# Optimization experiments

Measured on AMD Instinct MI355X. Metric: run time of the kernel, lower is better.

Reference implementation:

```python
import jax, jax.numpy as jnp
import numpy as np
import math

D_MODEL = 768
NUM_HEADS = 12
D_K = D_MODEL // NUM_HEADS

def setup_inputs() -> dict:
    key = jax.random.key(0)
    k_x, k_q, k_k, k_v, k_o = jax.random.split(key, 5)
    x = jax.random.normal(k_x, (2, 2048, D_MODEL), dtype=jnp.float32)
    std = math.sqrt(2.0 / (D_MODEL + D_MODEL))
    # trunc_normal approx: clip normal to [-3std, 3std]
    def tn(k):
        return jnp.clip(jax.random.normal(k, (D_MODEL, D_MODEL), dtype=jnp.float32) * std, -3 * std, 3 * std)
    return {
        "x": x,
        "weight_query": tn(k_q),
        "weight_key": tn(k_k),
        "weight_value": tn(k_v),
        "weight_output": tn(k_o),
    }

def reference(x, weight_query, weight_key, weight_value, weight_output):
    # x: (b, s, d_model); weights: (d_out, d_model)
    b, s, _ = x.shape
    def proj_heads(w):
        y = jnp.einsum('od,bsd->bso', w, x)  # (b, s, h*dk)
        return y.reshape(b, s, NUM_HEADS, D_K).transpose(0, 2, 1, 3)  # (b, h, s, dk)
    Q = proj_heads(weight_query)
    K = proj_heads(weight_key)
    V = proj_heads(weight_value)
    scores = jnp.einsum('bhqd,bhkd->bhqk', Q, K) / jnp.sqrt(jnp.asarray(D_K, x.dtype))
    causal = jnp.tril(jnp.ones((s, s), dtype=bool))  # (sq, sk)
    scores = jnp.where(causal, scores, -jnp.inf)
    attn = jax.nn.softmax(scores, axis=-1)
    out_heads = jnp.einsum('bhqk,bhkd->bhqd', attn, V)  # (b, h, s, dv)
    attn_out = out_heads.transpose(0, 2, 1, 3).reshape(b, s, NUM_HEADS * D_K)
    return jnp.einsum('di,bsi->bsd', weight_output, attn_out)
```

## Files before the change

kernel.cpp:

```cpp
#include <hip/hip_runtime.h>
#include <stdint.h>

typedef float f32x4 __attribute__((ext_vector_type(4)));
typedef __bf16 bf16x8 __attribute__((ext_vector_type(8)));
typedef uint32_t u32a  __attribute__((may_alias));
typedef uint2    u2a   __attribute__((may_alias));
typedef uint4    u4a   __attribute__((may_alias));

#define VS 2064

__device__ __forceinline__ ushort f2b(float f) {
  uint32_t u = __builtin_bit_cast(uint32_t, f);
  u += 0x7FFFu + ((u >> 16) & 1u);
  return (ushort)(u >> 16);
}
__device__ __forceinline__ uint32_t b16(uint32_t u) {
  u += 0x7FFFu + ((u >> 16) & 1u);
  return u >> 16;
}

__device__ __forceinline__ bf16x8 ld_frag(const ushort* p) {
  u4a u = *(const u4a*)p;
  return __builtin_bit_cast(bf16x8, u);
}

__device__ __forceinline__ u4a cvt8(const float* p) {
  u4a a = *(const u4a*)p, b = *(const u4a*)(p + 4), o;
  o.x = b16(a.x) | (b16(a.y) << 16);
  o.y = b16(a.z) | (b16(a.w) << 16);
  o.z = b16(b.x) | (b16(b.y) << 16);
  o.w = b16(b.z) | (b16(b.w) << 16);
  return o;
}

__device__ __forceinline__ void load_lds16(const void* g, void* l) {
  __builtin_amdgcn_global_load_lds(
      (const __attribute__((address_space(1))) uint32_t*)g,
      (__attribute__((address_space(3))) uint32_t*)l, 16, 0, 0);
}

__device__ __forceinline__ uint32_t comb2(uint32_t a, uint32_t b, float w0, float w1) {
  float lo = __builtin_bit_cast(float, a << 16) * w0 +
             __builtin_bit_cast(float, b << 16) * w1;
  float hi = __builtin_bit_cast(float, a & 0xFFFF0000u) * w0 +
             __builtin_bit_cast(float, b & 0xFFFF0000u) * w1;
  return (uint32_t)f2b(lo) | ((uint32_t)f2b(hi) << 16);
}

__global__ __launch_bounds__(256) void convert_kernel(
    const float* __restrict__ x,  const float* __restrict__ wq,
    const float* __restrict__ wk, const float* __restrict__ wv,
    const float* __restrict__ wo,
    ushort* __restrict__ xb,  ushort* __restrict__ wqb,
    ushort* __restrict__ wkb, ushort* __restrict__ wvb,
    ushort* __restrict__ wob)
{
  const size_t NX = 3145728, NW = 589824;
  size_t idx = ((size_t)blockIdx.x * 256 + threadIdx.x) * 8;
  const float* src; ushort* dst; size_t off;
  if      (idx < NX)          { src = x;  dst = xb;  off = idx; }
  else if (idx < NX + NW)     { src = wq; dst = wqb; off = idx - NX; }
  else if (idx < NX + 2 * NW) { src = wk; dst = wkb; off = idx - NX - NW; }
  else if (idx < NX + 3 * NW) { src = wv; dst = wvb; off = idx - NX - 2 * NW; }
  else                        { src = wo; dst = wob; off = idx - NX - 3 * NW; }
  *(u4a*)(dst + off) = cvt8(src + off);
}

__global__ __launch_bounds__(256) void gemm_qkv(
    const ushort* __restrict__ A,
    const ushort* __restrict__ B0, const ushort* __restrict__ B1,
    const ushort* __restrict__ B2,
    ushort* __restrict__ Qo, ushort* __restrict__ Ko, ushort* __restrict__ Vt,
    int M, int N, int K)
{
  const ushort* B = blockIdx.z == 0 ? B0 : (blockIdx.z == 1 ? B1 : B2);
  const int m0 = blockIdx.x * 128, n0 = blockIdx.y * 64;
  __shared__ ushort As[128 * 64];
  __shared__ ushort Bs[64 * 64];
  const int tid = threadIdx.x, wave = tid >> 6, lane = tid & 63;
  const int quad = lane >> 4, l16 = lane & 15;
  const int mw = (wave & 1) * 64, nw = (wave >> 1) * 32;
  f32x4 acc[4][2] = {};

  for (int k0 = 0; k0 < K; k0 += 64) {
#pragma unroll
    for (int i = 0; i < 4; ++i) {
      int c = i * 256 + tid;
      load_lds16(A + (size_t)(m0 + (c >> 3)) * K + k0 + (c & 7) * 8,
                 As + (size_t)(i * 256 + wave * 64) * 8);
    }
#pragma unroll
    for (int i = 0; i < 2; ++i) {
      int c = i * 256 + tid;
      load_lds16(B + (size_t)(n0 + (c >> 3)) * K + k0 + (c & 7) * 8,
                 Bs + (size_t)(i * 256 + wave * 64) * 8);
    }
    __syncthreads();
#pragma unroll
    for (int ks = 0; ks < 2; ++ks) {
      bf16x8 af[4], bfr[2];
#pragma unroll
      for (int i = 0; i < 4; ++i)
        af[i]  = ld_frag(As + (mw + i * 16 + l16) * 64 + ks * 32 + quad * 8);
#pragma unroll
      for (int j = 0; j < 2; ++j)
        bfr[j] = ld_frag(Bs + (nw + j * 16 + l16) * 64 + ks * 32 + quad * 8);
#pragma unroll
      for (int i = 0; i < 4; ++i)
#pragma unroll
        for (int j = 0; j < 2; ++j)
          acc[i][j] = __builtin_amdgcn_mfma_f32_16x16x32_bf16(af[i], bfr[j], acc[i][j], 0, 0, 0);
    }
    __syncthreads();
  }
  if (blockIdx.z < 2) {
    ushort* C = blockIdx.z == 0 ? Qo : Ko;
    const float sc = blockIdx.z == 0 ? 0.125f : 1.0f;
#pragma unroll
    for (int i = 0; i < 4; ++i)
#pragma unroll
      for (int j = 0; j < 2; ++j)
#pragma unroll
        for (int r = 0; r < 4; ++r) {
          int row = m0 + mw + i * 16 + quad * 4 + r;
          int col = n0 + nw + j * 16 + l16;
          C[(size_t)row * N + col] = f2b(acc[i][j][r] * sc);
        }
  } else {
#pragma unroll
    for (int i = 0; i < 4; ++i)
#pragma unroll
      for (int j = 0; j < 2; ++j) {
        int col = n0 + nw + j * 16 + l16;
        int h = col >> 6, dv = col & 63;
        int t = m0 + mw + i * 16 + quad * 4;
        int b = t >> 11, s = t & 2047;
        u2a pw;
        pw.x = (uint32_t)f2b(acc[i][j][0]) | ((uint32_t)f2b(acc[i][j][1]) << 16);
        pw.y = (uint32_t)f2b(acc[i][j][2]) | ((uint32_t)f2b(acc[i][j][3]) << 16);
        *(u2a*)(Vt + (((size_t)b * 12 + h) * 64 + dv) * VS + s) = pw;
      }
  }
}

__global__ __launch_bounds__(256) void gemm_out(
    const ushort* __restrict__ A, const ushort* __restrict__ B,
    float* __restrict__ C, int M, int N, int K)
{
  const int m0 = blockIdx.x * 64, n0 = blockIdx.y * 64;
  __shared__ ushort As[64 * 64];
  __shared__ ushort Bs[64 * 64];
  const int tid = threadIdx.x, wave = tid >> 6, lane = tid & 63;
  const int quad = lane >> 4, l16 = lane & 15;
  const int mw = (wave & 1) * 32, nw = (wave >> 1) * 32;
  f32x4 acc[2][2] = {};

  for (int k0 = 0; k0 < K; k0 += 64) {
#pragma unroll
    for (int i = 0; i < 2; ++i) {
      int c = i * 256 + tid;
      load_lds16(A + (size_t)(m0 + (c >> 3)) * K + k0 + (c & 7) * 8,
                 As + (size_t)(i * 256 + wave * 64) * 8);
      load_lds16(B + (size_t)(n0 + (c >> 3)) * K + k0 + (c & 7) * 8,
                 Bs + (size_t)(i * 256 + wave * 64) * 8);
    }
    __syncthreads();
#pragma unroll
    for (int ks = 0; ks < 2; ++ks) {
      bf16x8 af[2], bfr[2];
#pragma unroll
      for (int i = 0; i < 2; ++i)
        af[i]  = ld_frag(As + (mw + i * 16 + l16) * 64 + ks * 32 + quad * 8);
#pragma unroll
      for (int j = 0; j < 2; ++j)
        bfr[j] = ld_frag(Bs + (nw + j * 16 + l16) * 64 + ks * 32 + quad * 8);
#pragma unroll
      for (int i = 0; i < 2; ++i)
#pragma unroll
        for (int j = 0; j < 2; ++j)
          acc[i][j] = __builtin_amdgcn_mfma_f32_16x16x32_bf16(af[i], bfr[j], acc[i][j], 0, 0, 0);
    }
    __syncthreads();
  }
#pragma unroll
  for (int i = 0; i < 2; ++i)
#pragma unroll
    for (int j = 0; j < 2; ++j)
#pragma unroll
      for (int r = 0; r < 4; ++r) {
        int row = m0 + mw + i * 16 + quad * 4 + r;
        int col = n0 + nw + j * 16 + l16;
        C[(size_t)row * N + col] = acc[i][j][r];
      }
}

__global__ __launch_bounds__(256) void attn_kernel(
    const ushort* __restrict__ Qb, const ushort* __restrict__ Kb,
    const ushort* __restrict__ Vt, ushort* __restrict__ Opart,
    float2* __restrict__ MLp)
{
  const int S = 2048, DM = 768;
  const int pair = blockIdx.x >> 1, j = blockIdx.x & 1;
  const int h = blockIdx.y, bb = blockIdx.z;
  const ushort* Qp  = Qb + (size_t)bb * S * DM + h * 64;
  const ushort* Kp  = Kb + (size_t)bb * S * DM + h * 64;
  const ushort* Vth = Vt + ((size_t)bb * 12 + h) * 64 * VS;

  __shared__ ushort Ks[128 * 72];
  __shared__ ushort Vs[64 * 136];
  __shared__ ushort Ps[4][16 * 136];

  const int tid = threadIdx.x, wave = tid >> 6, lane = tid & 63;
  const int quad = lane >> 4, l16 = lane & 15;
  const float LOG2E = 1.44269504f;
  const float NEG_BIG = -1.0e30f;

  const int qtA = pair, qtB = 31 - pair;
  const int qgA = qtA * 64 + wave * 16 + l16;
  const int qgB = qtB * 64 + wave * 16 + l16;
  const int nktA = (qtA >> 1) + 1, nktB = (qtB >> 1) + 1;

  bf16x8 bqA0 = ld_frag(Qp + (size_t)qgA * DM + quad * 8);
  bf16x8 bqA1 = ld_frag(Qp + (size_t)qgA * DM + 32 + quad * 8);
  bf16x8 bqB0 = ld_frag(Qp + (size_t)qgB * DM + quad * 8);
  bf16x8 bqB1 = ld_frag(Qp + (size_t)qgB * DM + 32 + quad * 8);

  f32x4 accA[4] = {}, accB[4] = {};
  float mA = NEG_BIG, lA = 0.0f, mB = NEG_BIG, lB = 0.0f;

  for (int kt = j; kt < nktB; kt += 2) {
    const int kk0 = kt * 128;
#pragma unroll
    for (int i = 0; i < 4; ++i) {
      int c = i * 256 + tid;
      int r = c >> 3, col = (c & 7) * 8;
      *(u4a*)(Ks + r * 72 + col) = *(const u4a*)(Kp + (size_t)(kk0 + r) * DM + col);
    }
#pragma unroll
    for (int i = 0; i < 4; ++i) {
      int c = i * 256 + tid;
      int dv = c >> 4, kc = (c & 15) * 8;
      *(u4a*)(Vs + dv * 136 + kc) = *(const u4a*)(Vth + (size_t)dv * VS + kk0 + kc);
    }
    __syncthreads();

    auto strip = [&](const bf16x8& bq0, const bf16x8& bq1, f32x4* acc_o,
                     float& m_run, float& l_run, int qg, int nkt) {
      f32x4 sacc[8] = {};
#pragma unroll
      for (int tt = 0; tt < 8; ++tt) {
        bf16x8 ak0 = ld_frag(Ks + (tt * 16 + l16) * 72 + quad * 8);
        bf16x8 ak1 = ld_frag(Ks + (tt * 16 + l16) * 72 + 32 + quad * 8);
        sacc[tt] = __builtin_amdgcn_mfma_f32_16x16x32_bf16(ak0, bq0, sacc[tt], 0, 0, 0);
        sacc[tt] = __builtin_amdgcn_mfma_f32_16x16x32_bf16(ak1, bq1, sacc[tt], 0, 0, 0);
      }
      const bool domask = (kt == nkt - 1);
      float mt = NEG_BIG;
#pragma unroll
      for (int tt = 0; tt < 8; ++tt)
#pragma unroll
        for (int r = 0; r < 4; ++r) {
          float s = sacc[tt][r];
          if (domask) {
            int kkg = kk0 + tt * 16 + quad * 4 + r;
            if (kkg > qg) s = NEG_BIG;
          }
          sacc[tt][r] = s;
          mt = fmaxf(mt, s);
        }
      mt = fmaxf(mt, __shfl_xor(mt, 16, 64));
      mt = fmaxf(mt, __shfl_xor(mt, 32, 64));
      float mnew = fmaxf(m_run, mt);
      float alpha = exp2f((m_run - mnew) * LOG2E);
      float lsum = 0.0f;
#pragma unroll
      for (int tt = 0; tt < 8; ++tt) {
        float p0 = exp2f((sacc[tt][0] - mnew) * LOG2E);
        float p1 = exp2f((sacc[tt][1] - mnew) * LOG2E);
        float p2 = exp2f((sacc[tt][2] - mnew) * LOG2E);
        float p3 = exp2f((sacc[tt][3] - mnew) * LOG2E);
        lsum += (p0 + p1) + (p2 + p3);
        uint32_t u0 = __builtin_bit_cast(uint32_t, p0);
        uint32_t u1 = __builtin_bit_cast(uint32_t, p1);
        uint32_t u2 = __builtin_bit_cast(uint32_t, p2);
        uint32_t u3 = __builtin_bit_cast(uint32_t, p3);
        u2a pw;
        pw.x = (u0 >> 16) | (u1 & 0xFFFF0000u);
        pw.y = (u2 >> 16) | (u3 & 0xFFFF0000u);
        *(u2a*)(&Ps[wave][l16 * 136 + tt * 16 + quad * 4]) = pw;
      }
      asm volatile("s_waitcnt lgkmcnt(0)" ::: "memory");
      lsum += __shfl_xor(lsum, 16, 64);
      lsum += __shfl_xor(lsum, 32, 64);
      l_run = l_run * alpha + lsum;
      m_run = mnew;
      float ar0 = __shfl(alpha, quad * 4 + 0, 64);
      float ar1 = __shfl(alpha, quad * 4 + 1, 64);
      float ar2 = __shfl(alpha, quad * 4 + 2, 64);
      float ar3 = __shfl(alpha, quad * 4 + 3, 64);
#pragma unroll
      for (int ct = 0; ct < 4; ++ct) {
        acc_o[ct][0] *= ar0; acc_o[ct][1] *= ar1;
        acc_o[ct][2] *= ar2; acc_o[ct][3] *= ar3;
      }
#pragma unroll
      for (int ks = 0; ks < 4; ++ks) {
        bf16x8 ap = ld_frag(&Ps[wave][l16 * 136 + ks * 32 + quad * 8]);
#pragma unroll
        for (int ct = 0; ct < 4; ++ct) {
          bf16x8 bv = ld_frag(Vs + (size_t)(ct * 16 + l16) * 136 + ks * 32 + quad * 8);
          acc_o[ct] = __builtin_amdgcn_mfma_f32_16x16x32_bf16(ap, bv, acc_o[ct], 0, 0, 0);
        }
      }
    };

    strip(bqB0, bqB1, accB, mB, lB, qgB, nktB);
    if (kt < nktA)
      strip(bqA0, bqA1, accA, mA, lA, qgA, nktA);
    __syncthreads();
  }

  const int base = ((bb * 12 + h) << 5);
  const int r0 = wave * 16 + quad * 4;
  {
    const int slot = (base + qtB) * 2 + j;
    ushort* Os = Opart + (size_t)slot * 4096;
#pragma unroll
    for (int ct = 0; ct < 4; ++ct) {
      int col = ct * 16 + l16;
      Os[(r0 + 0) * 64 + col] = f2b(accB[ct][0]);
      Os[(r0 + 1) * 64 + col] = f2b(accB[ct][1]);
      Os[(r0 + 2) * 64 + col] = f2b(accB[ct][2]);
      Os[(r0 + 3) * 64 + col] = f2b(accB[ct][3]);
    }
    if (quad == 0)
      MLp[(size_t)slot * 64 + wave * 16 + l16] = make_float2(mB, lB);
  }
  {
    const int slot = (base + qtA) * 2 + j;
    ushort* Os = Opart + (size_t)slot * 4096;
#pragma unroll
    for (int ct = 0; ct < 4; ++ct) {
      int col = ct * 16 + l16;
      Os[(r0 + 0) * 64 + col] = f2b(accA[ct][0]);
      Os[(r0 + 1) * 64 + col] = f2b(accA[ct][1]);
      Os[(r0 + 2) * 64 + col] = f2b(accA[ct][2]);
      Os[(r0 + 3) * 64 + col] = f2b(accA[ct][3]);
    }
    if (quad == 0)
      MLp[(size_t)slot * 64 + wave * 16 + l16] = make_float2(mA, lA);
  }
}

__global__ __launch_bounds__(256) void combine_kernel(
    const ushort* __restrict__ Opart, const float2* __restrict__ MLp,
    ushort* __restrict__ Ab)
{
  const int sid = blockIdx.x;
  const int bb = sid / 384, rem = sid % 384, h = rem >> 5, qt = rem & 31;
  const int t = threadIdx.x, row = t >> 2, cg = (t & 3) * 16;
  float2 ml0 = MLp[(size_t)(sid * 2) * 64 + row];
  float2 ml1 = MLp[(size_t)(sid * 2 + 1) * 64 + row];
  float ms = fmaxf(ml0.x, ml1.x);
  float w0 = exp2f((ml0.x - ms) * 1.44269504f);
  float w1 = exp2f((ml1.x - ms) * 1.44269504f);
  float inv = 1.0f / (ml0.y * w0 + ml1.y * w1);
  w0 *= inv; w1 *= inv;
  const ushort* p0 = Opart + (size_t)(sid * 2) * 4096 + row * 64 + cg;
  ushort* dst = Ab + ((size_t)(bb * 2048 + qt * 64 + row)) * 768 + h * 64 + cg;
#pragma unroll
  for (int g = 0; g < 2; ++g) {
    u4a a = *(const u4a*)(p0 + g * 8);
    u4a b = *(const u4a*)(p0 + 4096 + g * 8);
    u4a o;
    o.x = comb2(a.x, b.x, w0, w1);
    o.y = comb2(a.y, b.y, w0, w1);
    o.z = comb2(a.z, b.z, w0, w1);
    o.w = comb2(a.w, b.w, w0, w1);
    *(u4a*)(dst + g * 8) = o;
  }
}

extern "C" void kernel_launch(void* const* d_in, const int* in_sizes, int n_in,
                              void* d_out, int out_size, void* d_ws, size_t ws_size,
                              hipStream_t stream) {
  (void)in_sizes; (void)n_in; (void)out_size; (void)ws_size;
  const float* x  = (const float*)d_in[0];
  const float* wq = (const float*)d_in[1];
  const float* wk = (const float*)d_in[2];
  const float* wv = (const float*)d_in[3];
  const float* wo = (const float*)d_in[4];

  const size_t NT = (size_t)4096 * 768;
  const size_t NW = (size_t)768 * 768;
  const size_t NV = (size_t)24 * 64 * VS;
  ushort* xb    = (ushort*)d_ws;
  ushort* Qbuf  = xb + NT;
  ushort* Kbuf  = Qbuf + NT;
  ushort* Vt    = Kbuf + NT;
  ushort* wqb   = Vt + NV;
  ushort* wkb   = wqb + NW;
  ushort* wvb   = wkb + NW;
  ushort* wob   = wvb + NW;
  ushort* Opart = wob + NW;
  float2* MLp   = (float2*)(Opart + (size_t)1536 * 4096);
  ushort* Abuf  = xb;

  convert_kernel<<<2688, 256, 0, stream>>>(x, wq, wk, wv, wo,
                                           xb, wqb, wkb, wvb, wob);
  gemm_qkv<<<dim3(32, 12, 3), 256, 0, stream>>>(
      xb, wqb, wkb, wvb, Qbuf, Kbuf, Vt, 4096, 768, 768);
  attn_kernel<<<dim3(32, 12, 2), 256, 0, stream>>>(Qbuf, Kbuf, Vt, Opart, MLp);
  combine_kernel<<<768, 256, 0, stream>>>(Opart, MLp, Abuf);
  gemm_out<<<dim3(64, 12), 256, 0, stream>>>(
      Abuf, wob, (float*)d_out, 4096, 768, 768);
}
```

Before: 173.6 us.

## Split attention KV four ways and keep P in registers

Attention work is split four ways over key tiles instead of two, doubling the block count, and the combine kernel merges four partials. The softmax probabilities stay in registers as the MFMA A operand, with V stored in LDS in a permuted column order to match; this removes the per-wave P staging in LDS and its wait. log2(e) is folded into the Q scale so the exponentials skip a multiply, and launch bounds request four blocks per CU. The cost is more partial-output traffic and a larger workspace.

Measured after the change: 325.3 us. +87.3%, slower.

```diff
diff --git a/kernel.cpp b/kernel.cpp
--- a/kernel.cpp
+++ b/kernel.cpp
@@ -39,11 +39,16 @@
       (__attribute__((address_space(3))) uint32_t*)l, 16, 0, 0);
 }
 
-__device__ __forceinline__ uint32_t comb2(uint32_t a, uint32_t b, float w0, float w1) {
+__device__ __forceinline__ uint32_t comb4(uint32_t a, uint32_t b, uint32_t c, uint32_t d,
+                                          float w0, float w1, float w2, float w3) {
   float lo = __builtin_bit_cast(float, a << 16) * w0 +
-             __builtin_bit_cast(float, b << 16) * w1;
+             __builtin_bit_cast(float, b << 16) * w1 +
+             __builtin_bit_cast(float, c << 16) * w2 +
+             __builtin_bit_cast(float, d << 16) * w3;
   float hi = __builtin_bit_cast(float, a & 0xFFFF0000u) * w0 +
-             __builtin_bit_cast(float, b & 0xFFFF0000u) * w1;
+             __builtin_bit_cast(float, b & 0xFFFF0000u) * w1 +
+             __builtin_bit_cast(float, c & 0xFFFF0000u) * w2 +
+             __builtin_bit_cast(float, d & 0xFFFF0000u) * w3;
   return (uint32_t)f2b(lo) | ((uint32_t)f2b(hi) << 16);
 }
 
@@ -115,7 +120,7 @@
   }
   if (blockIdx.z < 2) {
     ushort* C = blockIdx.z == 0 ? Qo : Ko;
-    const float sc = blockIdx.z == 0 ? 0.125f : 1.0f;
+    const float sc = blockIdx.z == 0 ? 0.18033688f : 1.0f;
 #pragma unroll
     for (int i = 0; i < 4; ++i)
 #pragma unroll
@@ -194,13 +199,13 @@
       }
 }
 
-__global__ __launch_bounds__(256) void attn_kernel(
+__global__ __launch_bounds__(256, 4) void attn_kernel(
     const ushort* __restrict__ Qb, const ushort* __restrict__ Kb,
     const ushort* __restrict__ Vt, ushort* __restrict__ Opart,
     float2* __restrict__ MLp)
 {
   const int S = 2048, DM = 768;
-  const int pair = blockIdx.x >> 1, j = blockIdx.x & 1;
+  const int pair = blockIdx.x >> 2, j = blockIdx.x & 3;
   const int h = blockIdx.y, bb = blockIdx.z;
   const ushort* Qp  = Qb + (size_t)bb * S * DM + h * 64;
   const ushort* Kp  = Kb + (size_t)bb * S * DM + h * 64;
@@ -208,11 +213,9 @@
 
   __shared__ ushort Ks[128 * 72];
   __shared__ ushort Vs[64 * 136];
-  __shared__ ushort Ps[4][16 * 136];
 
   const int tid = threadIdx.x, wave = tid >> 6, lane = tid & 63;
   const int quad = lane >> 4, l16 = lane & 15;
-  const float LOG2E = 1.44269504f;
   const float NEG_BIG = -1.0e30f;
 
   const int qtA = pair, qtB = 31 - pair;
@@ -228,7 +231,7 @@
   f32x4 accA[4] = {}, accB[4] = {};
   float mA = NEG_BIG, lA = 0.0f, mB = NEG_BIG, lB = 0.0f;
 
-  for (int kt = j; kt < nktB; kt += 2) {
+  for (int kt = j; kt < nktB; kt += 4) {
     const int kk0 = kt * 128;
 #pragma unroll
     for (int i = 0; i < 4; ++i) {
@@ -239,8 +242,13 @@
 #pragma unroll
     for (int i = 0; i < 4; ++i) {
       int c = i * 256 + tid;
-      int dv = c >> 4, kc = (c & 15) * 8;
-      *(u4a*)(Vs + dv * 136 + kc) = *(const u4a*)(Vth + (size_t)dv * VS + kk0 + kc);
+      int dv = c >> 4, kc8 = c & 15;
+      u4a g = *(const u4a*)(Vth + (size_t)dv * VS + kk0 + kc8 * 8);
+      int pos = ((kc8 >> 2) * 32) + ((kc8 & 1) * 16) + (((kc8 >> 1) & 1) * 4);
+      u2a lo, hi;
+      lo.x = g.x; lo.y = g.y; hi.x = g.z; hi.y = g.w;
+      *(u2a*)(Vs + dv * 136 + pos)     = lo;
+      *(u2a*)(Vs + dv * 136 + pos + 8) = hi;
     }
     __syncthreads();
 
@@ -271,25 +279,23 @@
       mt = fmaxf(mt, __shfl_xor(mt, 16, 64));
       mt = fmaxf(mt, __shfl_xor(mt, 32, 64));
       float mnew = fmaxf(m_run, mt);
-      float alpha = exp2f((m_run - mnew) * LOG2E);
+      float alpha = exp2f(m_run - mnew);
       float lsum = 0.0f;
+      uint32_t pp[16];
 #pragma unroll
       for (int tt = 0; tt < 8; ++tt) {
-        float p0 = exp2f((sacc[tt][0] - mnew) * LOG2E);
-        float p1 = exp2f((sacc[tt][1] - mnew) * LOG2E);
-        float p2 = exp2f((sacc[tt][2] - mnew) * LOG2E);
-        float p3 = exp2f((sacc[tt][3] - mnew) * LOG2E);
+        float p0 = exp2f(sacc[tt][0] - mnew);
+        float p1 = exp2f(sacc[tt][1] - mnew);
+        float p2 = exp2f(sacc[tt][2] - mnew);
+        float p3 = exp2f(sacc[tt][3] - mnew);
         lsum += (p0 + p1) + (p2 + p3);
         uint32_t u0 = __builtin_bit_cast(uint32_t, p0);
         uint32_t u1 = __builtin_bit_cast(uint32_t, p1);
         uint32_t u2 = __builtin_bit_cast(uint32_t, p2);
         uint32_t u3 = __builtin_bit_cast(uint32_t, p3);
-        u2a pw;
-        pw.x = (u0 >> 16) | (u1 & 0xFFFF0000u);
-        pw.y = (u2 >> 16) | (u3 & 0xFFFF0000u);
-        *(u2a*)(&Ps[wave][l16 * 136 + tt * 16 + quad * 4]) = pw;
-      }
-      asm volatile("s_waitcnt lgkmcnt(0)" ::: "memory");
+        pp[tt * 2]     = (u0 >> 16) | (u1 & 0xFFFF0000u);
+        pp[tt * 2 + 1] = (u2 >> 16) | (u3 & 0xFFFF0000u);
+      }
       lsum += __shfl_xor(lsum, 16, 64);
       lsum += __shfl_xor(lsum, 32, 64);
       l_run = l_run * alpha + lsum;
@@ -305,7 +311,10 @@
       }
 #pragma unroll
       for (int ks = 0; ks < 4; ++ks) {
-        bf16x8 ap = ld_frag(&Ps[wave][l16 * 136 + ks * 32 + quad * 8]);
+        u4a pu;
+        pu.x = pp[ks * 4];     pu.y = pp[ks * 4 + 1];
+        pu.z = pp[ks * 4 + 2]; pu.w = pp[ks * 4 + 3];
+        bf16x8 ap = __builtin_bit_cast(bf16x8, pu);
 #pragma unroll
         for (int ct = 0; ct < 4; ++ct) {
           bf16x8 bv = ld_frag(Vs + (size_t)(ct * 16 + l16) * 136 + ks * 32 + quad * 8);
@@ -323,7 +332,7 @@
   const int base = ((bb * 12 + h) << 5);
   const int r0 = wave * 16 + quad * 4;
   {
-    const int slot = (base + qtB) * 2 + j;
+    const int slot = (base + qtB) * 4 + j;
     ushort* Os = Opart + (size_t)slot * 4096;
 #pragma unroll
     for (int ct = 0; ct < 4; ++ct) {
@@ -337,7 +346,7 @@
       MLp[(size_t)slot * 64 + wave * 16 + l16] = make_float2(mB, lB);
   }
   {
-    const int slot = (base + qtA) * 2 + j;
+    const int slot = (base + qtA) * 4 + j;
     ushort* Os = Opart + (size_t)slot * 4096;
 #pragma unroll
     for (int ct = 0; ct < 4; ++ct) {
@@ -359,24 +368,30 @@
   const int sid = blockIdx.x;
   const int bb = sid / 384, rem = sid % 384, h = rem >> 5, qt = rem & 31;
   const int t = threadIdx.x, row = t >> 2, cg = (t & 3) * 16;
-  float2 ml0 = MLp[(size_t)(sid * 2) * 64 + row];
-  float2 ml1 = MLp[(size_t)(sid * 2 + 1) * 64 + row];
-  float ms = fmaxf(ml0.x, ml1.x);
-  float w0 = exp2f((ml0.x - ms) * 1.44269504f);
-  float w1 = exp2f((ml1.x - ms) * 1.44269504f);
-  float inv = 1.0f / (ml0.y * w0 + ml1.y * w1);
-  w0 *= inv; w1 *= inv;
-  const ushort* p0 = Opart + (size_t)(sid * 2) * 4096 + row * 64 + cg;
+  float2 ml0 = MLp[(size_t)(sid * 4 + 0) * 64 + row];
+  float2 ml1 = MLp[(size_t)(sid * 4 + 1) * 64 + row];
+  float2 ml2 = MLp[(size_t)(sid * 4 + 2) * 64 + row];
+  float2 ml3 = MLp[(size_t)(sid * 4 + 3) * 64 + row];
+  float ms = fmaxf(fmaxf(ml0.x, ml1.x), fmaxf(ml2.x, ml3.x));
+  float w0 = exp2f(ml0.x - ms);
+  float w1 = exp2f(ml1.x - ms);
+  float w2 = exp2f(ml2.x - ms);
+  float w3 = exp2f(ml3.x - ms);
+  float inv = 1.0f / (ml0.y * w0 + ml1.y * w1 + ml2.y * w2 + ml3.y * w3);
+  w0 *= inv; w1 *= inv; w2 *= inv; w3 *= inv;
+  const ushort* p0 = Opart + (size_t)(sid * 4) * 4096 + row * 64 + cg;
   ushort* dst = Ab + ((size_t)(bb * 2048 + qt * 64 + row)) * 768 + h * 64 + cg;
 #pragma unroll
   for (int g = 0; g < 2; ++g) {
     u4a a = *(const u4a*)(p0 + g * 8);
     u4a b = *(const u4a*)(p0 + 4096 + g * 8);
+    u4a c = *(const u4a*)(p0 + 8192 + g * 8);
+    u4a d = *(const u4a*)(p0 + 12288 + g * 8);
     u4a o;
-    o.x = comb2(a.x, b.x, w0, w1);
-    o.y = comb2(a.y, b.y, w0, w1);
-    o.z = comb2(a.z, b.z, w0, w1);
-    o.w = comb2(a.w, b.w, w0, w1);
+    o.x = comb4(a.x, b.x, c.x, d.x, w0, w1, w2, w3);
+    o.y = comb4(a.y, b.y, c.y, d.y, w0, w1, w2, w3);
+    o.z = comb4(a.z, b.z, c.z, d.z, w0, w1, w2, w3);
+    o.w = comb4(a.w, b.w, c.w, d.w, w0, w1, w2, w3);
     *(u4a*)(dst + g * 8) = o;
   }
 }
@@ -403,14 +418,14 @@
   ushort* wvb   = wkb + NW;
   ushort* wob   = wvb + NW;
   ushort* Opart = wob + NW;
-  float2* MLp   = (float2*)(Opart + (size_t)1536 * 4096);
+  float2* MLp   = (float2*)(Opart + (size_t)3072 * 4096);
   ushort* Abuf  = xb;
 
   convert_kernel<<<2688, 256, 0, stream>>>(x, wq, wk, wv, wo,
                                            xb, wqb, wkb, wvb, wob);
   gemm_qkv<<<dim3(32, 12, 3), 256, 0, stream>>>(
       xb, wqb, wkb, wvb, Qbuf, Kbuf, Vt, 4096, 768, 768);
-  attn_kernel<<<dim3(32, 12, 2), 256, 0, stream>>>(Qbuf, Kbuf, Vt, Opart, MLp);
+  attn_kernel<<<dim3(64, 12, 2), 256, 0, stream>>>(Qbuf, Kbuf, Vt, Opart, MLp);
   combine_kernel<<<768, 256, 0, stream>>>(Opart, MLp, Abuf);
   gemm_out<<<dim3(64, 12), 256, 0, stream>>>(
       Abuf, wob, (float*)d_out, 4096, 768, 768);
```
